# Kernel optimization log

Hardware: AMD Instinct MI355X
Metric: run time of the kernel (lower is better)

## Reference

```python
import jax, jax.numpy as jnp
import numpy as np


def setup_inputs() -> dict:
    key = jax.random.key(0)
    k1, k2, k3 = jax.random.split(key, 3)
    B, S, H = 32, 2048, 1024
    hidden = jax.random.normal(k1, (B, H), dtype=jnp.float32)
    encoder_outputs = jax.random.normal(k2, (B, S, H), dtype=jnp.float32)
    W_in = jax.random.normal(k3, (H, H), dtype=jnp.float32) * (1.0 / np.sqrt(H))
    return {"hidden": hidden, "encoder_outputs": encoder_outputs, "W_in": W_in}


def reference(hidden, encoder_outputs, W_in):
    # linear_in: nn.Linear(H, H, bias=False) -> hidden @ W_in.T  [B, H]
    h = hidden @ W_in.T
    # scores: bmm(encoder_outputs [B,S,H], h [B,H,1]) -> [B,S]
    scores = jnp.einsum("bsh,bh->bs", encoder_outputs, h)
    attn_w = jax.nn.softmax(scores, axis=-1)  # [B, S]
    # context: bmm(attn_w [B,1,S], encoder_outputs [B,S,H]) -> [B, H]
    context = jnp.einsum("bs,bsh->bh", attn_w, encoder_outputs)
    return (context, attn_w)
```

## Files before the change

kernel.cpp:

```cpp
#include <hip/hip_runtime.h>
#include <math.h>

constexpr int Bb = 32;
constexpr int Ss = 2048;
constexpr int Hh = 1024;
constexpr int SC = 64;
constexpr int CPB = Ss / SC;
constexpr int NBLK = Bb * CPB;

__global__ __launch_bounds__(256) void gemv_h_kernel(const float* __restrict__ hidden,
                                                     const float* __restrict__ W,
                                                     float* __restrict__ h)
{
    int tid  = threadIdx.x;
    int wave = tid >> 6;
    int lane = tid & 63;
    int i  = blockIdx.x >> 3;
    int bg = blockIdx.x & 7;
    int b  = bg * 4 + wave;
    const float4* wr = reinterpret_cast<const float4*>(W + (size_t)i * Hh);
    const float4* hd = reinterpret_cast<const float4*>(hidden + (size_t)b * Hh);
    float d = 0.f;
#pragma unroll
    for (int k = 0; k < 4; ++k) {
        float4 wv = wr[lane + 64 * k];
        float4 hv = hd[lane + 64 * k];
        d += wv.x * hv.x + wv.y * hv.y + wv.z * hv.z + wv.w * hv.w;
    }
#pragma unroll
    for (int off = 32; off > 0; off >>= 1) d += __shfl_xor(d, off, 64);
    if (lane == 0) h[(size_t)b * Hh + i] = d;
}

__global__ __launch_bounds__(256) void attn_partial_kernel(const float* __restrict__ enc,
                                                           const float* __restrict__ h,
                                                           float* __restrict__ scores,
                                                           float* __restrict__ pm,
                                                           float* __restrict__ pl,
                                                           float* __restrict__ pctx)
{
    int blk   = blockIdx.x;
    int b     = blk / CPB;
    int chunk = blk % CPB;
    int s0    = chunk * SC;
    int tid   = threadIdx.x;
    int wave  = tid >> 6;
    int lane  = tid & 63;

    float4 hf[4];
    const float4* h4 = reinterpret_cast<const float4*>(h + (size_t)b * Hh);
#pragma unroll
    for (int k = 0; k < 4; ++k) hf[k] = h4[lane + 64 * k];

    float m = -INFINITY;
    float l = 0.f;
    float4 ctx[4];
#pragma unroll
    for (int k = 0; k < 4; ++k) ctx[k] = make_float4(0.f, 0.f, 0.f, 0.f);

    for (int r = 0; r < 16; ++r) {
        int s = s0 + wave * 16 + r;
        const float4* e4 = reinterpret_cast<const float4*>(enc + ((size_t)b * Ss + s) * Hh);
        float4 ev[4];
#pragma unroll
        for (int k = 0; k < 4; ++k) ev[k] = e4[lane + 64 * k];
        float d = 0.f;
#pragma unroll
        for (int k = 0; k < 4; ++k)
            d += ev[k].x * hf[k].x + ev[k].y * hf[k].y + ev[k].z * hf[k].z + ev[k].w * hf[k].w;
#pragma unroll
        for (int off = 32; off > 0; off >>= 1) d += __shfl_xor(d, off, 64);
        if (lane == 0) scores[(size_t)b * Ss + s] = d;

        if (d > m) {
            float c = __expf(m - d);
            l *= c;
#pragma unroll
            for (int k = 0; k < 4; ++k) {
                ctx[k].x *= c; ctx[k].y *= c; ctx[k].z *= c; ctx[k].w *= c;
            }
            m = d;
        }
        float p = __expf(d - m);
        l += p;
#pragma unroll
        for (int k = 0; k < 4; ++k) {
            ctx[k].x += p * ev[k].x; ctx[k].y += p * ev[k].y;
            ctx[k].z += p * ev[k].z; ctx[k].w += p * ev[k].w;
        }
    }

    __shared__ float lds_ctx[4][Hh];
    __shared__ float lds_m[4], lds_l[4];
    float4* ldsrow = reinterpret_cast<float4*>(lds_ctx[wave]);
#pragma unroll
    for (int k = 0; k < 4; ++k) ldsrow[64 * k + lane] = ctx[k];
    if (lane == 0) { lds_m[wave] = m; lds_l[wave] = l; }
    __syncthreads();

    float M = fmaxf(fmaxf(lds_m[0], lds_m[1]), fmaxf(lds_m[2], lds_m[3]));
    float L = 0.f;
    float4 acc = make_float4(0.f, 0.f, 0.f, 0.f);
#pragma unroll
    for (int w = 0; w < 4; ++w) {
        float c = __expf(lds_m[w] - M);
        L += c * lds_l[w];
        float4 v = reinterpret_cast<float4*>(lds_ctx[w])[tid];
        acc.x += c * v.x; acc.y += c * v.y; acc.z += c * v.z; acc.w += c * v.w;
    }
    reinterpret_cast<float4*>(pctx + (size_t)blk * Hh)[tid] = acc;
    if (tid == 0) { pm[blk] = M; pl[blk] = L; }
}

__global__ __launch_bounds__(256) void combine_kernel(const float* __restrict__ pm,
                                                      const float* __restrict__ pl,
                                                      const float* __restrict__ pctx,
                                                      float* __restrict__ out_ctx,
                                                      float* __restrict__ Mb,
                                                      float* __restrict__ Lb)
{
    int b   = blockIdx.x >> 2;
    int j   = blockIdx.x & 3;
    int tid = threadIdx.x;
    int col = j * 256 + tid;

    const float* mrow = pm + (size_t)b * CPB;
    const float* lrow = pl + (size_t)b * CPB;

    float M = -INFINITY;
#pragma unroll
    for (int c = 0; c < CPB; ++c) M = fmaxf(M, mrow[c]);
    float e[CPB];
    float L = 0.f;
#pragma unroll
    for (int c = 0; c < CPB; ++c) {
        e[c] = __expf(mrow[c] - M);
        L += e[c] * lrow[c];
    }
    float acc = 0.f;
#pragma unroll 4
    for (int c = 0; c < CPB; ++c)
        acc += e[c] * pctx[((size_t)b * CPB + c) * Hh + col];
    out_ctx[(size_t)b * Hh + col] = acc / L;
    if (j == 0 && tid == 0) { Mb[b] = M; Lb[b] = L; }
}

__global__ __launch_bounds__(256) void finish_attn_kernel(const float* __restrict__ scores,
                                                          const float* __restrict__ Mb,
                                                          const float* __restrict__ Lb,
                                                          float* __restrict__ attn_out)
{
    int idx = blockIdx.x * 256 + threadIdx.x;
    int b = idx >> 11;
    float inv = 1.f / Lb[b];
    attn_out[idx] = __expf(scores[idx] - Mb[b]) * inv;
}

extern "C" void kernel_launch(void* const* d_in, const int* in_sizes, int n_in,
                              void* d_out, int out_size, void* d_ws, size_t ws_size,
                              hipStream_t stream) {
    const float* hidden = (const float*)d_in[0];
    const float* enc    = (const float*)d_in[1];
    const float* W_in   = (const float*)d_in[2];

    float* out_ctx  = (float*)d_out;
    float* out_attn = (float*)d_out + Bb * Hh;

    float* ws     = (float*)d_ws;
    float* h      = ws;
    float* scores = ws + 32768;
    float* pm     = ws + 98304;
    float* pl     = ws + 99328;
    float* pctx   = ws + 100352;
    float* Mb     = pctx + (size_t)NBLK * Hh;
    float* Lb     = Mb + Bb;
    (void)in_sizes; (void)n_in; (void)out_size; (void)ws_size;

    gemv_h_kernel<<<Hh * (Bb / 4), 256, 0, stream>>>(hidden, W_in, h);
    attn_partial_kernel<<<NBLK, 256, 0, stream>>>(enc, h, scores, pm, pl, pctx);
    combine_kernel<<<Bb * (Hh / 256), 256, 0, stream>>>(pm, pl, pctx, out_ctx, Mb, Lb);
    finish_attn_kernel<<<(Bb * Ss) / 256, 256, 0, stream>>>(scores, Mb, Lb, out_attn);
}
```

Measured before the change: 68.55 us.

## Fuse combine and finish kernels, process two rows per iteration, remap gemv blocks

The combine and attention-normalisation kernels are merged into a single launch, with each finish block recomputing the per-batch max and sum from the partial stats. This removes one kernel launch and the Mb/Lb round trip. The partial attention loop now handles two encoder rows per iteration, giving more loads in flight and fewer online-softmax rescales. The gemv block index mapping is changed so consecutive blocks walk W rows for the same batch group. The cost is redundant max/exp work in each finish block.

```diff
diff --git a/kernel.cpp b/kernel.cpp
--- a/kernel.cpp
+++ b/kernel.cpp
@@ -15,8 +15,8 @@
     int tid  = threadIdx.x;
     int wave = tid >> 6;
     int lane = tid & 63;
-    int i  = blockIdx.x >> 3;
-    int bg = blockIdx.x & 7;
+    int i  = blockIdx.x & (Hh - 1);
+    int bg = blockIdx.x >> 10;
     int b  = bg * 4 + wave;
     const float4* wr = reinterpret_cast<const float4*>(W + (size_t)i * Hh);
     const float4* hd = reinterpret_cast<const float4*>(hidden + (size_t)b * Hh);
@@ -58,35 +58,53 @@
 #pragma unroll
     for (int k = 0; k < 4; ++k) ctx[k] = make_float4(0.f, 0.f, 0.f, 0.f);
 
-    for (int r = 0; r < 16; ++r) {
-        int s = s0 + wave * 16 + r;
-        const float4* e4 = reinterpret_cast<const float4*>(enc + ((size_t)b * Ss + s) * Hh);
-        float4 ev[4];
+    const float4* ebase = reinterpret_cast<const float4*>(enc + ((size_t)b * Ss + s0 + wave * 16) * Hh);
+
+#pragma unroll 2
+    for (int r2 = 0; r2 < 8; ++r2) {
+        const float4* eA = ebase + (size_t)(2 * r2) * (Hh / 4);
+        const float4* eB = eA + (Hh / 4);
+        float4 ea[4], eb[4];
 #pragma unroll
-        for (int k = 0; k < 4; ++k) ev[k] = e4[lane + 64 * k];
-        float d = 0.f;
+        for (int k = 0; k < 4; ++k) ea[k] = eA[lane + 64 * k];
 #pragma unroll
-        for (int k = 0; k < 4; ++k)
-            d += ev[k].x * hf[k].x + ev[k].y * hf[k].y + ev[k].z * hf[k].z + ev[k].w * hf[k].w;
+        for (int k = 0; k < 4; ++k) eb[k] = eB[lane + 64 * k];
+
+        float d0 = 0.f, d1 = 0.f;
 #pragma unroll
-        for (int off = 32; off > 0; off >>= 1) d += __shfl_xor(d, off, 64);
-        if (lane == 0) scores[(size_t)b * Ss + s] = d;
+        for (int k = 0; k < 4; ++k) {
+            d0 += ea[k].x * hf[k].x + ea[k].y * hf[k].y + ea[k].z * hf[k].z + ea[k].w * hf[k].w;
+            d1 += eb[k].x * hf[k].x + eb[k].y * hf[k].y + eb[k].z * hf[k].z + eb[k].w * hf[k].w;
+        }
+#pragma unroll
+        for (int off = 32; off > 0; off >>= 1) {
+            d0 += __shfl_xor(d0, off, 64);
+            d1 += __shfl_xor(d1, off, 64);
+        }
+        int s = s0 + wave * 16 + 2 * r2;
+        if (lane == 0) {
+            *reinterpret_cast<float2*>(scores + (size_t)b * Ss + s) = make_float2(d0, d1);
+        }
 
-        if (d > m) {
-            float c = __expf(m - d);
+        float mn = fmaxf(fmaxf(d0, d1), m);
+        if (mn > m) {
+            float c = __expf(m - mn);
             l *= c;
 #pragma unroll
             for (int k = 0; k < 4; ++k) {
                 ctx[k].x *= c; ctx[k].y *= c; ctx[k].z *= c; ctx[k].w *= c;
             }
-            m = d;
+            m = mn;
         }
-        float p = __expf(d - m);
-        l += p;
+        float p0 = __expf(d0 - m);
+        float p1 = __expf(d1 - m);
+        l += p0 + p1;
 #pragma unroll
         for (int k = 0; k < 4; ++k) {
-            ctx[k].x += p * ev[k].x; ctx[k].y += p * ev[k].y;
-            ctx[k].z += p * ev[k].z; ctx[k].w += p * ev[k].w;
+            ctx[k].x += p0 * ea[k].x + p1 * eb[k].x;
+            ctx[k].y += p0 * ea[k].y + p1 * eb[k].y;
+            ctx[k].z += p0 * ea[k].z + p1 * eb[k].z;
+            ctx[k].w += p0 * ea[k].w + p1 * eb[k].w;
         }
     }
 
@@ -112,48 +130,48 @@
     if (tid == 0) { pm[blk] = M; pl[blk] = L; }
 }
 
-__global__ __launch_bounds__(256) void combine_kernel(const float* __restrict__ pm,
-                                                      const float* __restrict__ pl,
-                                                      const float* __restrict__ pctx,
-                                                      float* __restrict__ out_ctx,
-                                                      float* __restrict__ Mb,
-                                                      float* __restrict__ Lb)
+__global__ __launch_bounds__(256) void combine_finish_kernel(const float* __restrict__ pm,
+                                                             const float* __restrict__ pl,
+                                                             const float* __restrict__ pctx,
+                                                             const float* __restrict__ scores,
+                                                             float* __restrict__ out_ctx,
+                                                             float* __restrict__ attn_out)
 {
-    int b   = blockIdx.x >> 2;
-    int j   = blockIdx.x & 3;
+    int blk = blockIdx.x;
     int tid = threadIdx.x;
-    int col = j * 256 + tid;
-
-    const float* mrow = pm + (size_t)b * CPB;
-    const float* lrow = pl + (size_t)b * CPB;
-
-    float M = -INFINITY;
+    if (blk < 128) {
+        int b = blk >> 2;
+        int col = (blk & 3) * 256 + tid;
+        const float* mrow = pm + (size_t)b * CPB;
+        const float* lrow = pl + (size_t)b * CPB;
+        float M = -INFINITY;
 #pragma unroll
-    for (int c = 0; c < CPB; ++c) M = fmaxf(M, mrow[c]);
-    float e[CPB];
-    float L = 0.f;
+        for (int c = 0; c < CPB; ++c) M = fmaxf(M, mrow[c]);
+        float e[CPB];
+        float L = 0.f;
 #pragma unroll
-    for (int c = 0; c < CPB; ++c) {
-        e[c] = __expf(mrow[c] - M);
-        L += e[c] * lrow[c];
+        for (int c = 0; c < CPB; ++c) {
+            e[c] = __expf(mrow[c] - M);
+            L += e[c] * lrow[c];
+        }
+        float acc = 0.f;
+#pragma unroll 4
+        for (int c = 0; c < CPB; ++c)
+            acc += e[c] * pctx[((size_t)b * CPB + c) * Hh + col];
+        out_ctx[(size_t)b * Hh + col] = acc / L;
+    } else {
+        int idx = (blk - 128) * 256 + tid;
+        int b = idx >> 11;
+        const float* mrow = pm + (size_t)b * CPB;
+        const float* lrow = pl + (size_t)b * CPB;
+        float M = -INFINITY;
+#pragma unroll
+        for (int c = 0; c < CPB; ++c) M = fmaxf(M, mrow[c]);
+        float L = 0.f;
+#pragma unroll
+        for (int c = 0; c < CPB; ++c) L += __expf(mrow[c] - M) * lrow[c];
+        attn_out[idx] = __expf(scores[idx] - M) / L;
     }
-    float acc = 0.f;
-#pragma unroll 4
-    for (int c = 0; c < CPB; ++c)
-        acc += e[c] * pctx[((size_t)b * CPB + c) * Hh + col];
-    out_ctx[(size_t)b * Hh + col] = acc / L;
-    if (j == 0 && tid == 0) { Mb[b] = M; Lb[b] = L; }
-}
-
-__global__ __launch_bounds__(256) void finish_attn_kernel(const float* __restrict__ scores,
-                                                          const float* __restrict__ Mb,
-                                                          const float* __restrict__ Lb,
-                                                          float* __restrict__ attn_out)
-{
-    int idx = blockIdx.x * 256 + threadIdx.x;
-    int b = idx >> 11;
-    float inv = 1.f / Lb[b];
-    attn_out[idx] = __expf(scores[idx] - Mb[b]) * inv;
 }
 
 extern "C" void kernel_launch(void* const* d_in, const int* in_sizes, int n_in,
@@ -172,12 +190,10 @@
     float* pm     = ws + 98304;
     float* pl     = ws + 99328;
     float* pctx   = ws + 100352;
-    float* Mb     = pctx + (size_t)NBLK * Hh;
-    float* Lb     = Mb + Bb;
     (void)in_sizes; (void)n_in; (void)out_size; (void)ws_size;
 
     gemv_h_kernel<<<Hh * (Bb / 4), 256, 0, stream>>>(hidden, W_in, h);
     attn_partial_kernel<<<NBLK, 256, 0, stream>>>(enc, h, scores, pm, pl, pctx);
-    combine_kernel<<<Bb * (Hh / 256), 256, 0, stream>>>(pm, pl, pctx, out_ctx, Mb, Lb);
-    finish_attn_kernel<<<(Bb * Ss) / 256, 256, 0, stream>>>(scores, Mb, Lb, out_attn);
+    combine_finish_kernel<<<128 + (Bb * Ss) / 256, 256, 0, stream>>>(pm, pl, pctx, scores,
+                                                                     out_ctx, out_attn);
 }
```

New measurement: 64.03 us. 6.6% less time.
